# Kernel optimization log

Hardware: AMD Instinct MI355X
Metric: run time of the kernel (lower is better)

The kernel has to match this reference:

```python
import jax, jax.numpy as jnp
import numpy as np

B = 256   # batch size
NX = 256  # spatial grid points
T = 100   # time steps in u
TEMP = 1.0
LAM = 0.9  # lambda_1


def _advection(u, dt, dx, coeff):
    d = (jnp.roll(u, 1, axis=1) - jnp.roll(u, -1, axis=1)) * u
    return coeff[:, None, None] * dt[:, None, None] * d / (2.0 * dx[:, None, None])


def _diffusion(u, dt, dx, coeff):
    d = jnp.roll(u, 1, axis=1) + jnp.roll(u, -1, axis=1) - 2.0 * u
    return -(coeff[:, None, None] * dt[:, None, None] * d / dx[:, None, None] ** 2)


def _linear_advection(u, dt, dx, coeff):
    num = u - jnp.roll(u, -1, axis=1)
    return -coeff[:, None, None] * dt[:, None, None] * num / dx[:, None, None]


def _anchored_l2(xi, xj, ui, uj, dt, dx, coeff):
    # us[i, j, :] = ui[j, :, -1] - uj[i, :, -2]  -> [2B, 2B, NX]
    us = ui[..., -1][None, :, :] - uj[..., -2][:, None, :]
    adv = _advection(xi, dt, dx, coeff[:, 0])
    diff = _diffusion(xi, dt, dx, coeff[:, 1])
    dis = _linear_advection(xi, dt, dx, coeff[:, 2])
    updates = (adv + diff + dis)[..., 0]  # [2B, NX]
    pd = (xi[..., 0] + updates)[:, None, :] - xj[..., 0][None, :, :]  # [2B, 2B, NX]
    d = us - pd
    return jnp.sum(d * d, axis=-1)  # norm(dim=-1)**2


def reference(x1, x2, u, dt, dx, vs):
    bs = x1.shape[0]
    # _pde_similarity(vs): pairwise sqrt(sum|vi*vj|) / max(||vi||, ||vj||)
    prod = jnp.sqrt(jnp.sum(jnp.abs(vs[None, :, :] * vs[:, None, :]), axis=-1))
    nv = jnp.linalg.norm(vs, axis=-1)
    sim = prod / jnp.maximum(nv[:, None], nv[None, :])
    ss = jnp.nan_to_num(1.0 - LAM * sim, nan=0.0)
    # drop diagonal (row-major, static indices), then tile to [2B, 2(B-1)]
    ri, ci = np.nonzero(~np.eye(bs, dtype=bool))
    ss = ss[ri, ci].reshape(bs, bs - 1)
    ss = jnp.tile(ss, (2, 2))
    reps = jnp.concatenate([x2, x1], axis=0)           # [2B, NX, 1, 1]
    reps = reps.reshape(2 * bs, -1, reps.shape[-1])    # flatten(1,2) -> [2B, NX, 1]
    u2 = jnp.concatenate([u, u], axis=0)
    dt2 = jnp.concatenate([dt, dt], axis=0)
    vs2 = jnp.concatenate([vs, vs], axis=0)
    simmat = _anchored_l2(reps, reps, u2, u2, dt2, dx, vs2)  # [2B, 2B]
    l_pos = jnp.diagonal(simmat, offset=bs)
    r_pos = jnp.diagonal(simmat, offset=-bs)
    pos = jnp.concatenate([l_pos, r_pos]).reshape(2 * bs, 1)
    m = np.eye(2 * bs) + np.eye(2 * bs, k=-bs) + np.eye(2 * bs, k=bs)
    nri, nci = np.nonzero((1 - m).astype(bool))
    neg = simmat[nri, nci].reshape(2 * bs, 2 * bs - 2) * ss
    logits = jnp.concatenate([pos, neg], axis=1) / TEMP
    lp = jax.nn.log_softmax(logits, axis=-1)
    # CrossEntropyLoss(reduction='sum') with all labels == 0
    return -jnp.sum(lp[:, 0]) / (2 * bs)


def setup_inputs():
    key = jax.random.key(0)
    k1, k2, k3, k4, k5 = jax.random.split(key, 5)
    return {
        'x1': jax.random.normal(k1, (B, NX, 1, 1), dtype=jnp.float32),
        'x2': jax.random.normal(k2, (B, NX, 1, 1), dtype=jnp.float32),
        'u': jax.random.normal(k3, (B, NX, T), dtype=jnp.float32),
        'dt': jax.random.uniform(k4, (B,), dtype=jnp.float32),
        'dx': jnp.ones((1,), dtype=jnp.float32),
        'vs': jax.random.normal(k5, (B, 3), dtype=jnp.float32),
    }
```

## Files before the change

### kernel.cpp

```cpp
#include <hip/hip_runtime.h>
#include <math.h>

#define BQ 256
#define NXQ 256
#define TQ 100
#define N2 512
#define TILE 32
#define PITCH 257

__global__ __launch_bounds__(256) void prep_kernel(
    const float* __restrict__ x1, const float* __restrict__ x2,
    const float* __restrict__ u, const float* __restrict__ dt,
    const float* __restrict__ dx, const float* __restrict__ vs,
    float* __restrict__ A, float* __restrict__ C) {
  int b = blockIdx.x;
  int t = threadIdx.x;
  __shared__ float w2s[NXQ], w1s[NXQ];
  float w2 = x2[b * NXQ + t];
  float w1 = x1[b * NXQ + t];
  w2s[t] = w2;
  w1s[t] = w1;
  float2 uv = *(const float2*)(u + (size_t)(b * NXQ + t) * TQ + (TQ - 2));
  float dtv = dt[b];
  float dxv = dx[0];
  float c0 = vs[b * 3 + 0], c1 = vs[b * 3 + 1], c2 = vs[b * 3 + 2];
  __syncthreads();
  int tm = (t + NXQ - 1) & (NXQ - 1);
  int tp = (t + 1) & (NXQ - 1);
  float w2m = w2s[tm], w2p = w2s[tp];
  float w1m = w1s[tm], w1p = w1s[tp];
  float adv2 = c0 * dtv * (w2m - w2p) * w2 / (2.0f * dxv);
  float dif2 = -(c1 * dtv * (w2m + w2p - 2.0f * w2) / (dxv * dxv));
  float dis2 = -c2 * dtv * (w2 - w2p) / dxv;
  float adv1 = c0 * dtv * (w1m - w1p) * w1 / (2.0f * dxv);
  float dif1 = -(c1 * dtv * (w1m + w1p - 2.0f * w1) / (dxv * dxv));
  float dis1 = -c2 * dtv * (w1 - w1p) / dxv;
  A[b * NXQ + t] = uv.y + w2;
  A[(b + BQ) * NXQ + t] = uv.y + w1;
  C[b * NXQ + t] = uv.x + w2 + (adv2 + dif2 + dis2);
  C[(b + BQ) * NXQ + t] = uv.x + w1 + (adv1 + dif1 + dis1);
}

__global__ __launch_bounds__(256) void dist_kernel(const float* __restrict__ A,
                                                   const float* __restrict__ C,
                                                   float* __restrict__ SIM) {
  __shared__ float At[TILE * PITCH];
  __shared__ float Ct[TILE * PITCH];
  int t = threadIdx.x;
  int i0 = blockIdx.y * TILE;
  int j0 = blockIdx.x * TILE;
  for (int k = 0; k < TILE * NXQ / 256; k++) {
    int idx = k * 256 + t;
    int row = idx >> 8;
    int col = idx & (NXQ - 1);
    At[row * PITCH + col] = A[(j0 + row) * NXQ + col];
    Ct[row * PITCH + col] = C[(i0 + row) * NXQ + col];
  }
  __syncthreads();
  int ii = t >> 3;
  int jj = (t & 7) << 2;
  float acc0 = 0.f, acc1 = 0.f, acc2 = 0.f, acc3 = 0.f;
  for (int x = 0; x < NXQ; x++) {
    float cv = Ct[ii * PITCH + x];
    float d0 = At[(jj + 0) * PITCH + x] - cv;
    float d1 = At[(jj + 1) * PITCH + x] - cv;
    float d2 = At[(jj + 2) * PITCH + x] - cv;
    float d3 = At[(jj + 3) * PITCH + x] - cv;
    acc0 = fmaf(d0, d0, acc0);
    acc1 = fmaf(d1, d1, acc1);
    acc2 = fmaf(d2, d2, acc2);
    acc3 = fmaf(d3, d3, acc3);
  }
  float4 v = make_float4(acc0, acc1, acc2, acc3);
  *(float4*)&SIM[(i0 + ii) * N2 + j0 + jj] = v;
}

__global__ __launch_bounds__(256) void row_kernel(const float* __restrict__ SIM,
                                                  const float* __restrict__ vs,
                                                  double* __restrict__ ROW) {
  int r = blockIdx.x;
  int t = threadIdx.x;
  int rb = r & (BQ - 1);
  float vi0 = vs[rb * 3], vi1 = vs[rb * 3 + 1], vi2 = vs[rb * 3 + 2];
  float vj0 = vs[t * 3], vj1 = vs[t * 3 + 1], vj2 = vs[t * 3 + 2];
  float nvi = sqrtf(vi0 * vi0 + vi1 * vi1 + vi2 * vi2);
  float nvj = sqrtf(vj0 * vj0 + vj1 * vj1 + vj2 * vj2);
  float prod = sqrtf(fabsf(vi0 * vj0) + fabsf(vi1 * vj1) + fabsf(vi2 * vj2));
  float sim = prod / fmaxf(nvi, nvj);
  float ssv = 1.0f - 0.9f * sim;
  if (isnan(ssv)) ssv = 0.0f;

  int jstar = (r + BQ) & (N2 - 1);
  float posval = SIM[r * N2 + jstar];
  float v0, v1;
  {
    int j = t;
    if (j == jstar)                v0 = posval;
    else if ((j & (BQ - 1)) == rb) v0 = -INFINITY;
    else                           v0 = SIM[r * N2 + j] * ssv;
  }
  {
    int j = t + BQ;
    if (j == jstar)                v1 = posval;
    else if ((j & (BQ - 1)) == rb) v1 = -INFINITY;
    else                           v1 = SIM[r * N2 + j] * ssv;
  }
  float m = fmaxf(v0, v1);
  for (int off = 32; off > 0; off >>= 1) m = fmaxf(m, __shfl_down(m, off, 64));
  __shared__ float wmax[4];
  __shared__ double wsum[4];
  int wave = t >> 6, lane = t & 63;
  if (lane == 0) wmax[wave] = m;
  __syncthreads();
  float M = fmaxf(fmaxf(wmax[0], wmax[1]), fmaxf(wmax[2], wmax[3]));
  double s = 0.0;
  if (v0 != -INFINITY) s += exp((double)(v0 - M));
  if (v1 != -INFINITY) s += exp((double)(v1 - M));
  for (int off = 32; off > 0; off >>= 1) s += __shfl_down(s, off, 64);
  if (lane == 0) wsum[wave] = s;
  __syncthreads();
  if (t == 0) {
    double S = wsum[0] + wsum[1] + wsum[2] + wsum[3];
    ROW[r] = (double)M + log(S) - (double)posval;
  }
}

__global__ __launch_bounds__(256) void final_kernel(const double* __restrict__ ROW,
                                                    float* __restrict__ out) {
  int t = threadIdx.x;
  double s = ROW[t] + ROW[t + 256];
  for (int off = 32; off > 0; off >>= 1) s += __shfl_down(s, off, 64);
  __shared__ double wsum[4];
  int wave = t >> 6, lane = t & 63;
  if (lane == 0) wsum[wave] = s;
  __syncthreads();
  if (t == 0) {
    double S = wsum[0] + wsum[1] + wsum[2] + wsum[3];
    out[0] = (float)(S / (double)N2);
  }
}

extern "C" void kernel_launch(void* const* d_in, const int* in_sizes, int n_in,
                              void* d_out, int out_size, void* d_ws, size_t ws_size,
                              hipStream_t stream) {
  const float* x1 = (const float*)d_in[0];
  const float* x2 = (const float*)d_in[1];
  const float* u  = (const float*)d_in[2];
  const float* dt = (const float*)d_in[3];
  const float* dx = (const float*)d_in[4];
  const float* vs = (const float*)d_in[5];
  char* ws = (char*)d_ws;
  float*  SIM = (float*)(ws + 0);
  float*  A   = (float*)(ws + 1048576);
  float*  C   = (float*)(ws + 1572864);
  double* ROW = (double*)(ws + 2097152);
  float* out = (float*)d_out;

  prep_kernel<<<BQ, 256, 0, stream>>>(x1, x2, u, dt, dx, vs, A, C);
  dim3 g2(N2 / TILE, N2 / TILE);
  dist_kernel<<<g2, 256, 0, stream>>>(A, C, SIM);
  row_kernel<<<N2, 256, 0, stream>>>(SIM, vs, ROW);
  final_kernel<<<1, 256, 0, stream>>>(ROW, out);
}
```

Baseline: 93.81 us.

## Fuse prep stage into distance kernel, computing A/C tiles on the fly

Removes the separate prep kernel and the A/C workspace buffers; each distance tile block now builds its A and C rows directly from x1/x2, u, dt and vs while filling shared memory. This saves one launch and a global write/read round trip of the intermediate arrays. The cost is redundant recomputation: every tile block reloads its rows and gathers single strided elements of u (stride T floats), so u and x are reread 16 times across blocks, with uncoalesced access to u.

New measurement: 108.6 us. 1.16x slower.

```diff
diff --git a/kernel.cpp b/kernel.cpp
--- a/kernel.cpp
+++ b/kernel.cpp
@@ -8,53 +8,40 @@
 #define TILE 32
 #define PITCH 257
 
-__global__ __launch_bounds__(256) void prep_kernel(
+__global__ __launch_bounds__(256) void dist_kernel(
     const float* __restrict__ x1, const float* __restrict__ x2,
     const float* __restrict__ u, const float* __restrict__ dt,
     const float* __restrict__ dx, const float* __restrict__ vs,
-    float* __restrict__ A, float* __restrict__ C) {
-  int b = blockIdx.x;
-  int t = threadIdx.x;
-  __shared__ float w2s[NXQ], w1s[NXQ];
-  float w2 = x2[b * NXQ + t];
-  float w1 = x1[b * NXQ + t];
-  w2s[t] = w2;
-  w1s[t] = w1;
-  float2 uv = *(const float2*)(u + (size_t)(b * NXQ + t) * TQ + (TQ - 2));
-  float dtv = dt[b];
-  float dxv = dx[0];
-  float c0 = vs[b * 3 + 0], c1 = vs[b * 3 + 1], c2 = vs[b * 3 + 2];
-  __syncthreads();
-  int tm = (t + NXQ - 1) & (NXQ - 1);
-  int tp = (t + 1) & (NXQ - 1);
-  float w2m = w2s[tm], w2p = w2s[tp];
-  float w1m = w1s[tm], w1p = w1s[tp];
-  float adv2 = c0 * dtv * (w2m - w2p) * w2 / (2.0f * dxv);
-  float dif2 = -(c1 * dtv * (w2m + w2p - 2.0f * w2) / (dxv * dxv));
-  float dis2 = -c2 * dtv * (w2 - w2p) / dxv;
-  float adv1 = c0 * dtv * (w1m - w1p) * w1 / (2.0f * dxv);
-  float dif1 = -(c1 * dtv * (w1m + w1p - 2.0f * w1) / (dxv * dxv));
-  float dis1 = -c2 * dtv * (w1 - w1p) / dxv;
-  A[b * NXQ + t] = uv.y + w2;
-  A[(b + BQ) * NXQ + t] = uv.y + w1;
-  C[b * NXQ + t] = uv.x + w2 + (adv2 + dif2 + dis2);
-  C[(b + BQ) * NXQ + t] = uv.x + w1 + (adv1 + dif1 + dis1);
-}
-
-__global__ __launch_bounds__(256) void dist_kernel(const float* __restrict__ A,
-                                                   const float* __restrict__ C,
-                                                   float* __restrict__ SIM) {
+    float* __restrict__ SIM) {
   __shared__ float At[TILE * PITCH];
   __shared__ float Ct[TILE * PITCH];
   int t = threadIdx.x;
   int i0 = blockIdx.y * TILE;
   int j0 = blockIdx.x * TILE;
-  for (int k = 0; k < TILE * NXQ / 256; k++) {
-    int idx = k * 256 + t;
-    int row = idx >> 8;
-    int col = idx & (NXQ - 1);
-    At[row * PITCH + col] = A[(j0 + row) * NXQ + col];
-    Ct[row * PITCH + col] = C[(i0 + row) * NXQ + col];
+  const float* __restrict__ xA = (j0 < BQ) ? x2 : x1;
+  const float* __restrict__ xC = (i0 < BQ) ? x2 : x1;
+  int bA0 = j0 & (BQ - 1);
+  int bC0 = i0 & (BQ - 1);
+  float dxv = dx[0];
+  int tm = (t + NXQ - 1) & (NXQ - 1);
+  int tp = (t + 1) & (NXQ - 1);
+#pragma unroll 4
+  for (int it = 0; it < TILE; ++it) {
+    int bA = bA0 + it;
+    float wA = xA[bA * NXQ + t];
+    float uy = u[(size_t)(bA * NXQ + t) * TQ + (TQ - 1)];
+    At[it * PITCH + t] = uy + wA;
+    int bC = bC0 + it;
+    float wC = xC[bC * NXQ + t];
+    float wCm = xC[bC * NXQ + tm];
+    float wCp = xC[bC * NXQ + tp];
+    float ux = u[(size_t)(bC * NXQ + t) * TQ + (TQ - 2)];
+    float dtv = dt[bC];
+    float c0 = vs[bC * 3 + 0], c1 = vs[bC * 3 + 1], c2 = vs[bC * 3 + 2];
+    float adv = c0 * dtv * (wCm - wCp) * wC / (2.0f * dxv);
+    float dif = -(c1 * dtv * (wCm + wCp - 2.0f * wC) / (dxv * dxv));
+    float dis = -c2 * dtv * (wC - wCp) / dxv;
+    Ct[it * PITCH + t] = ux + wC + (adv + dif + dis);
   }
   __syncthreads();
   int ii = t >> 3;
@@ -151,14 +138,11 @@
   const float* vs = (const float*)d_in[5];
   char* ws = (char*)d_ws;
   float*  SIM = (float*)(ws + 0);
-  float*  A   = (float*)(ws + 1048576);
-  float*  C   = (float*)(ws + 1572864);
-  double* ROW = (double*)(ws + 2097152);
+  double* ROW = (double*)(ws + 1048576);
   float* out = (float*)d_out;
 
-  prep_kernel<<<BQ, 256, 0, stream>>>(x1, x2, u, dt, dx, vs, A, C);
   dim3 g2(N2 / TILE, N2 / TILE);
-  dist_kernel<<<g2, 256, 0, stream>>>(A, C, SIM);
+  dist_kernel<<<g2, 256, 0, stream>>>(x1, x2, u, dt, dx, vs, SIM);
   row_kernel<<<N2, 256, 0, stream>>>(SIM, vs, ROW);
   final_kernel<<<1, 256, 0, stream>>>(ROW, out);
 }
```

## Fuse all four kernels into one cooperative kernel with grid syncs

Applied to the files above, without the earlier changes.

Merges the prep, pairwise distance, row log-softmax and final reduction kernels into a single cooperative launch of 256 blocks, with grid-wide barriers between phases. The goal is to remove three kernel launches and the gaps between them. Each block now handles one distance tile and two softmax rows. The cost is grid-sync overhead, and the large shared-memory footprint must still let all 256 blocks be co-resident.

Measured after the change: 188.0 us. 2x slower.

```diff
diff --git a/kernel.cpp b/kernel.cpp
--- a/kernel.cpp
+++ b/kernel.cpp
@@ -1,5 +1,8 @@
 #include <hip/hip_runtime.h>
+#include <hip/hip_cooperative_groups.h>
 #include <math.h>
+
+namespace cg = cooperative_groups;
 
 #define BQ 256
 #define NXQ 256
@@ -8,135 +11,138 @@
 #define TILE 32
 #define PITCH 257
 
-__global__ __launch_bounds__(256) void prep_kernel(
+__global__ __launch_bounds__(256) void fused_all(
     const float* __restrict__ x1, const float* __restrict__ x2,
     const float* __restrict__ u, const float* __restrict__ dt,
     const float* __restrict__ dx, const float* __restrict__ vs,
-    float* __restrict__ A, float* __restrict__ C) {
-  int b = blockIdx.x;
-  int t = threadIdx.x;
-  __shared__ float w2s[NXQ], w1s[NXQ];
-  float w2 = x2[b * NXQ + t];
-  float w1 = x1[b * NXQ + t];
-  w2s[t] = w2;
-  w1s[t] = w1;
-  float2 uv = *(const float2*)(u + (size_t)(b * NXQ + t) * TQ + (TQ - 2));
-  float dtv = dt[b];
-  float dxv = dx[0];
-  float c0 = vs[b * 3 + 0], c1 = vs[b * 3 + 1], c2 = vs[b * 3 + 2];
-  __syncthreads();
-  int tm = (t + NXQ - 1) & (NXQ - 1);
-  int tp = (t + 1) & (NXQ - 1);
-  float w2m = w2s[tm], w2p = w2s[tp];
-  float w1m = w1s[tm], w1p = w1s[tp];
-  float adv2 = c0 * dtv * (w2m - w2p) * w2 / (2.0f * dxv);
-  float dif2 = -(c1 * dtv * (w2m + w2p - 2.0f * w2) / (dxv * dxv));
-  float dis2 = -c2 * dtv * (w2 - w2p) / dxv;
-  float adv1 = c0 * dtv * (w1m - w1p) * w1 / (2.0f * dxv);
-  float dif1 = -(c1 * dtv * (w1m + w1p - 2.0f * w1) / (dxv * dxv));
-  float dis1 = -c2 * dtv * (w1 - w1p) / dxv;
-  A[b * NXQ + t] = uv.y + w2;
-  A[(b + BQ) * NXQ + t] = uv.y + w1;
-  C[b * NXQ + t] = uv.x + w2 + (adv2 + dif2 + dis2);
-  C[(b + BQ) * NXQ + t] = uv.x + w1 + (adv1 + dif1 + dis1);
-}
-
-__global__ __launch_bounds__(256) void dist_kernel(const float* __restrict__ A,
-                                                   const float* __restrict__ C,
-                                                   float* __restrict__ SIM) {
+    float* __restrict__ A, float* __restrict__ C,
+    float* __restrict__ SIM, double* __restrict__ ROW,
+    float* __restrict__ out) {
+  cg::grid_group grid = cg::this_grid();
   __shared__ float At[TILE * PITCH];
   __shared__ float Ct[TILE * PITCH];
-  int t = threadIdx.x;
-  int i0 = blockIdx.y * TILE;
-  int j0 = blockIdx.x * TILE;
-  for (int k = 0; k < TILE * NXQ / 256; k++) {
-    int idx = k * 256 + t;
-    int row = idx >> 8;
-    int col = idx & (NXQ - 1);
-    At[row * PITCH + col] = A[(j0 + row) * NXQ + col];
-    Ct[row * PITCH + col] = C[(i0 + row) * NXQ + col];
-  }
-  __syncthreads();
-  int ii = t >> 3;
-  int jj = (t & 7) << 2;
-  float acc0 = 0.f, acc1 = 0.f, acc2 = 0.f, acc3 = 0.f;
-  for (int x = 0; x < NXQ; x++) {
-    float cv = Ct[ii * PITCH + x];
-    float d0 = At[(jj + 0) * PITCH + x] - cv;
-    float d1 = At[(jj + 1) * PITCH + x] - cv;
-    float d2 = At[(jj + 2) * PITCH + x] - cv;
-    float d3 = At[(jj + 3) * PITCH + x] - cv;
-    acc0 = fmaf(d0, d0, acc0);
-    acc1 = fmaf(d1, d1, acc1);
-    acc2 = fmaf(d2, d2, acc2);
-    acc3 = fmaf(d3, d3, acc3);
-  }
-  float4 v = make_float4(acc0, acc1, acc2, acc3);
-  *(float4*)&SIM[(i0 + ii) * N2 + j0 + jj] = v;
-}
-
-__global__ __launch_bounds__(256) void row_kernel(const float* __restrict__ SIM,
-                                                  const float* __restrict__ vs,
-                                                  double* __restrict__ ROW) {
-  int r = blockIdx.x;
-  int t = threadIdx.x;
-  int rb = r & (BQ - 1);
-  float vi0 = vs[rb * 3], vi1 = vs[rb * 3 + 1], vi2 = vs[rb * 3 + 2];
-  float vj0 = vs[t * 3], vj1 = vs[t * 3 + 1], vj2 = vs[t * 3 + 2];
-  float nvi = sqrtf(vi0 * vi0 + vi1 * vi1 + vi2 * vi2);
-  float nvj = sqrtf(vj0 * vj0 + vj1 * vj1 + vj2 * vj2);
-  float prod = sqrtf(fabsf(vi0 * vj0) + fabsf(vi1 * vj1) + fabsf(vi2 * vj2));
-  float sim = prod / fmaxf(nvi, nvj);
-  float ssv = 1.0f - 0.9f * sim;
-  if (isnan(ssv)) ssv = 0.0f;
-
-  int jstar = (r + BQ) & (N2 - 1);
-  float posval = SIM[r * N2 + jstar];
-  float v0, v1;
-  {
-    int j = t;
-    if (j == jstar)                v0 = posval;
-    else if ((j & (BQ - 1)) == rb) v0 = -INFINITY;
-    else                           v0 = SIM[r * N2 + j] * ssv;
-  }
-  {
-    int j = t + BQ;
-    if (j == jstar)                v1 = posval;
-    else if ((j & (BQ - 1)) == rb) v1 = -INFINITY;
-    else                           v1 = SIM[r * N2 + j] * ssv;
-  }
-  float m = fmaxf(v0, v1);
-  for (int off = 32; off > 0; off >>= 1) m = fmaxf(m, __shfl_down(m, off, 64));
   __shared__ float wmax[4];
   __shared__ double wsum[4];
-  int wave = t >> 6, lane = t & 63;
-  if (lane == 0) wmax[wave] = m;
-  __syncthreads();
-  float M = fmaxf(fmaxf(wmax[0], wmax[1]), fmaxf(wmax[2], wmax[3]));
-  double s = 0.0;
-  if (v0 != -INFINITY) s += exp((double)(v0 - M));
-  if (v1 != -INFINITY) s += exp((double)(v1 - M));
-  for (int off = 32; off > 0; off >>= 1) s += __shfl_down(s, off, 64);
-  if (lane == 0) wsum[wave] = s;
-  __syncthreads();
-  if (t == 0) {
-    double S = wsum[0] + wsum[1] + wsum[2] + wsum[3];
-    ROW[r] = (double)M + log(S) - (double)posval;
+  int g = blockIdx.x;
+  int t = threadIdx.x;
+
+  {
+    float* w2s = At;
+    float* w1s = Ct;
+    int b = g;
+    float w2 = x2[b * NXQ + t];
+    float w1 = x1[b * NXQ + t];
+    w2s[t] = w2;
+    w1s[t] = w1;
+    float2 uv = *(const float2*)(u + (size_t)(b * NXQ + t) * TQ + (TQ - 2));
+    float dtv = dt[b];
+    float dxv = dx[0];
+    float c0 = vs[b * 3 + 0], c1 = vs[b * 3 + 1], c2 = vs[b * 3 + 2];
+    __syncthreads();
+    int tm = (t + NXQ - 1) & (NXQ - 1);
+    int tp = (t + 1) & (NXQ - 1);
+    float w2m = w2s[tm], w2p = w2s[tp];
+    float w1m = w1s[tm], w1p = w1s[tp];
+    float adv2 = c0 * dtv * (w2m - w2p) * w2 / (2.0f * dxv);
+    float dif2 = -(c1 * dtv * (w2m + w2p - 2.0f * w2) / (dxv * dxv));
+    float dis2 = -c2 * dtv * (w2 - w2p) / dxv;
+    float adv1 = c0 * dtv * (w1m - w1p) * w1 / (2.0f * dxv);
+    float dif1 = -(c1 * dtv * (w1m + w1p - 2.0f * w1) / (dxv * dxv));
+    float dis1 = -c2 * dtv * (w1 - w1p) / dxv;
+    A[b * NXQ + t] = uv.y + w2;
+    A[(b + BQ) * NXQ + t] = uv.y + w1;
+    C[b * NXQ + t] = uv.x + w2 + (adv2 + dif2 + dis2);
+    C[(b + BQ) * NXQ + t] = uv.x + w1 + (adv1 + dif1 + dis1);
   }
-}
+  grid.sync();
 
-__global__ __launch_bounds__(256) void final_kernel(const double* __restrict__ ROW,
-                                                    float* __restrict__ out) {
-  int t = threadIdx.x;
-  double s = ROW[t] + ROW[t + 256];
-  for (int off = 32; off > 0; off >>= 1) s += __shfl_down(s, off, 64);
-  __shared__ double wsum[4];
-  int wave = t >> 6, lane = t & 63;
-  if (lane == 0) wsum[wave] = s;
-  __syncthreads();
-  if (t == 0) {
-    double S = wsum[0] + wsum[1] + wsum[2] + wsum[3];
-    out[0] = (float)(S / (double)N2);
+  {
+    int i0 = (g >> 4) * TILE;
+    int j0 = (g & 15) * TILE;
+    for (int k = 0; k < TILE * NXQ / 256; k++) {
+      int idx = k * 256 + t;
+      int row = idx >> 8;
+      int col = idx & (NXQ - 1);
+      At[row * PITCH + col] = A[(j0 + row) * NXQ + col];
+      Ct[row * PITCH + col] = C[(i0 + row) * NXQ + col];
+    }
+    __syncthreads();
+    int ii = t >> 3;
+    int jj = (t & 7) << 2;
+    float acc0 = 0.f, acc1 = 0.f, acc2 = 0.f, acc3 = 0.f;
+    for (int x = 0; x < NXQ; x++) {
+      float cv = Ct[ii * PITCH + x];
+      float d0 = At[(jj + 0) * PITCH + x] - cv;
+      float d1 = At[(jj + 1) * PITCH + x] - cv;
+      float d2 = At[(jj + 2) * PITCH + x] - cv;
+      float d3 = At[(jj + 3) * PITCH + x] - cv;
+      acc0 = fmaf(d0, d0, acc0);
+      acc1 = fmaf(d1, d1, acc1);
+      acc2 = fmaf(d2, d2, acc2);
+      acc3 = fmaf(d3, d3, acc3);
+    }
+    float4 v = make_float4(acc0, acc1, acc2, acc3);
+    *(float4*)&SIM[(i0 + ii) * N2 + j0 + jj] = v;
+  }
+  grid.sync();
+
+  for (int rr = 0; rr < 2; rr++) {
+    int r = g + rr * BQ;
+    int rb = r & (BQ - 1);
+    float vi0 = vs[rb * 3], vi1 = vs[rb * 3 + 1], vi2 = vs[rb * 3 + 2];
+    float vj0 = vs[t * 3], vj1 = vs[t * 3 + 1], vj2 = vs[t * 3 + 2];
+    float nvi = sqrtf(vi0 * vi0 + vi1 * vi1 + vi2 * vi2);
+    float nvj = sqrtf(vj0 * vj0 + vj1 * vj1 + vj2 * vj2);
+    float prod = sqrtf(fabsf(vi0 * vj0) + fabsf(vi1 * vj1) + fabsf(vi2 * vj2));
+    float sim = prod / fmaxf(nvi, nvj);
+    float ssv = 1.0f - 0.9f * sim;
+    if (isnan(ssv)) ssv = 0.0f;
+
+    int jstar = (r + BQ) & (N2 - 1);
+    float posval = SIM[r * N2 + jstar];
+    float v0, v1;
+    {
+      int j = t;
+      if (j == jstar)                v0 = posval;
+      else if ((j & (BQ - 1)) == rb) v0 = -INFINITY;
+      else                           v0 = SIM[r * N2 + j] * ssv;
+    }
+    {
+      int j = t + BQ;
+      if (j == jstar)                v1 = posval;
+      else if ((j & (BQ - 1)) == rb) v1 = -INFINITY;
+      else                           v1 = SIM[r * N2 + j] * ssv;
+    }
+    float m = fmaxf(v0, v1);
+    for (int off = 32; off > 0; off >>= 1) m = fmaxf(m, __shfl_down(m, off, 64));
+    int wave = t >> 6, lane = t & 63;
+    if (lane == 0) wmax[wave] = m;
+    __syncthreads();
+    float M = fmaxf(fmaxf(wmax[0], wmax[1]), fmaxf(wmax[2], wmax[3]));
+    double s = 0.0;
+    if (v0 != -INFINITY) s += exp((double)(v0 - M));
+    if (v1 != -INFINITY) s += exp((double)(v1 - M));
+    for (int off = 32; off > 0; off >>= 1) s += __shfl_down(s, off, 64);
+    if (lane == 0) wsum[wave] = s;
+    __syncthreads();
+    if (t == 0) {
+      double S = wsum[0] + wsum[1] + wsum[2] + wsum[3];
+      ROW[r] = (double)M + log(S) - (double)posval;
+    }
+    __syncthreads();
+  }
+  grid.sync();
+
+  if (g == 0) {
+    double s = ROW[t] + ROW[t + 256];
+    for (int off = 32; off > 0; off >>= 1) s += __shfl_down(s, off, 64);
+    int wave = t >> 6, lane = t & 63;
+    if (lane == 0) wsum[wave] = s;
+    __syncthreads();
+    if (t == 0) {
+      double S = wsum[0] + wsum[1] + wsum[2] + wsum[3];
+      out[0] = (float)(S / (double)N2);
+    }
   }
 }
 
@@ -156,9 +162,9 @@
   double* ROW = (double*)(ws + 2097152);
   float* out = (float*)d_out;
 
-  prep_kernel<<<BQ, 256, 0, stream>>>(x1, x2, u, dt, dx, vs, A, C);
-  dim3 g2(N2 / TILE, N2 / TILE);
-  dist_kernel<<<g2, 256, 0, stream>>>(A, C, SIM);
-  row_kernel<<<N2, 256, 0, stream>>>(SIM, vs, ROW);
-  final_kernel<<<1, 256, 0, stream>>>(ROW, out);
+  void* args[] = {(void*)&x1, (void*)&x2, (void*)&u,   (void*)&dt,
+                  (void*)&dx, (void*)&vs, (void*)&A,   (void*)&C,
+                  (void*)&SIM, (void*)&ROW, (void*)&out};
+  hipLaunchCooperativeKernel((const void*)fused_all, dim3(BQ), dim3(256), args, 0,
+                             stream);
 }
```
